# Optimization experiments

Hardware: AMD Instinct MI355X
Metric: run time of the kernel (lower is better)

Reference implementation:

```python
import jax, jax.numpy as jnp
import numpy as np

IN_FEATURES = 128
OUT_FEATURES = 64
NEG_INF = -9e15
LEAKY_SLOPE = 0.01  # nn.LeakyReLU() default


def _xavier_uniform(key, shape, gain):
    fan_in, fan_out = shape[0], shape[1]
    limit = gain * np.sqrt(6.0 / (fan_in + fan_out))
    return jax.random.uniform(key, shape, jnp.float32, -limit, limit)


def setup_inputs() -> dict:
    key = jax.random.key(0)
    k_h, k_adj, k_w, k_a = jax.random.split(key, 4)
    B, N = 8, 2048
    h = jax.random.normal(k_h, (B, N, IN_FEATURES), dtype=jnp.float32)
    adj = jax.random.randint(k_adj, (B, N, N), 0, 2, dtype=jnp.int32)
    W = _xavier_uniform(k_w, (IN_FEATURES, OUT_FEATURES), gain=1.414)
    a = _xavier_uniform(k_a, (2 * OUT_FEATURES, 1), gain=1.414)
    return {"h": h, "adj": adj, "W": W, "a": a}


def reference(h, adj, W, a):
    # Wh: [B, N, out]
    Wh = jnp.matmul(h, W)
    # a1, a2: [out, 1] slices of a
    a1 = a[:OUT_FEATURES]
    a2 = a[OUT_FEATURES:]
    Wh_a1 = jnp.matmul(Wh, a1)  # [B, N, 1]
    Wh_a2 = jnp.matmul(Wh, a2)  # [B, N, 1]
    # e[b,i,j] = leakyrelu(Wh_a1[b,i] * Wh_a2[b,j])  -- rank-1 outer product
    e = jax.nn.leaky_relu(Wh_a1 * jnp.swapaxes(Wh_a2, 1, 2), negative_slope=LEAKY_SLOPE)
    mask = adj > 0
    attention = jnp.where(mask, e, NEG_INF)
    attention = jax.nn.softmax(attention, axis=2)
    attention = jnp.where(mask, attention, 0.0)
    h_prime = jnp.matmul(attention, Wh)  # [B, N, out]
    return jax.nn.elu(h_prime)  # concat=True
```

## Files before the change

kernel.cpp:

```cpp
#include <hip/hip_runtime.h>

#define NTOK 2048

typedef __attribute__((ext_vector_type(8))) short s8v;
typedef __attribute__((ext_vector_type(4))) float f32x4;

__device__ inline unsigned short f2bf(float f) {
  unsigned u = __builtin_bit_cast(unsigned, f);
  u += 0x7FFFu + ((u >> 16) & 1u);
  return (unsigned short)(u >> 16);
}

__global__ __launch_bounds__(256) void gat_pre(
    const float* __restrict__ h, const float* __restrict__ W,
    const float* __restrict__ a, unsigned short* __restrict__ WhT,
    float* __restrict__ f1, float* __restrict__ f2,
    float* __restrict__ gmaxs, float* __restrict__ gmins) {
  __shared__ float wL[128 * 64];
  __shared__ float hL[64 * 128];
  __shared__ unsigned short tL[64 * 66];
  __shared__ float bmx[4], bmn[4];
  int t = threadIdx.x;
  {
    const float4* W4 = (const float4*)W;
    float4* wL4 = (float4*)wL;
#pragma unroll
    for (int k = 0; k < 8; ++k) wL4[t + 256 * k] = W4[t + 256 * k];
    const float4* h4 = (const float4*)(h + (size_t)blockIdx.x * 64 * 128);
    float4* hL4 = (float4*)hL;
#pragma unroll
    for (int k = 0; k < 8; ++k) hL4[t + 256 * k] = h4[t + 256 * k];
  }
  __syncthreads();
  int w = t >> 6, lane = t & 63;
  float acc[16];
#pragma unroll
  for (int r = 0; r < 16; ++r) acc[r] = 0.f;
  for (int kc = 0; kc < 128; kc += 32) {
    float wreg[32];
#pragma unroll
    for (int kk = 0; kk < 32; ++kk) wreg[kk] = wL[(kc + kk) * 64 + lane];
#pragma unroll
    for (int r = 0; r < 16; ++r) {
      const float* hrow = &hL[(w * 16 + r) * 128 + kc];
#pragma unroll
      for (int kk = 0; kk < 32; kk += 4) {
        float4 hv = *(const float4*)(hrow + kk);
        acc[r] += hv.x * wreg[kk] + hv.y * wreg[kk + 1] +
                  hv.z * wreg[kk + 2] + hv.w * wreg[kk + 3];
      }
    }
  }
  float a1 = a[lane], a2 = a[lane + 64];
  int row0 = blockIdx.x * 64 + w * 16;
  float wmx = -3.4e38f, wmn = 3.4e38f;
#pragma unroll
  for (int r = 0; r < 16; ++r) {
    float v1 = acc[r] * a1, v2 = acc[r] * a2;
#pragma unroll
    for (int s = 32; s; s >>= 1) {
      v1 += __shfl_xor(v1, s, 64);
      v2 += __shfl_xor(v2, s, 64);
    }
    if (lane == 0) { f1[row0 + r] = v1; f2[row0 + r] = v2; }
    wmx = fmaxf(wmx, v2);
    wmn = fminf(wmn, v2);
    tL[lane * 66 + w * 16 + r] = f2bf(acc[r]);
  }
  if (lane == 0) { bmx[w] = wmx; bmn[w] = wmn; }
  __syncthreads();
  int b = blockIdx.x >> 5;
  if (t == 0) {
    float mx = fmaxf(fmaxf(bmx[0], bmx[1]), fmaxf(bmx[2], bmx[3]));
    float mn = fminf(fminf(bmn[0], bmn[1]), fminf(bmn[2], bmn[3]));
    gmaxs[b * 32 + (blockIdx.x & 31)] = mx;
    gmins[b * 32 + (blockIdx.x & 31)] = mn;
  }
  int tok0 = (blockIdx.x & 31) * 64;
  int f = t >> 2, sub = t & 3;
  const unsigned short* src = &tL[f * 66];
  unsigned short* dst = WhT + ((size_t)b * 64 + f) * NTOK + tok0;
  *(uint4*)(dst + sub * 8) = *(const uint4*)(src + sub * 8);
  *(uint4*)(dst + 32 + sub * 8) = *(const uint4*)(src + 32 + sub * 8);
}

#define LOADX4(dst, va) \
  asm volatile("global_load_dwordx4 %0, %1, off" : "=v"(dst) : "v"(va))
#define WAITV(n) \
  asm volatile("s_waitcnt vmcnt(" #n ")" ::: "memory"); \
  __builtin_amdgcn_sched_barrier(0)
#define PACK4(s0, s1, s2, s3, s4, s5, s6, s7, D)                               \
  {                                                                            \
    unsigned b0 = (unsigned)(s0.x > 0) | ((unsigned)(s0.y > 0) << 1) |         \
                  ((unsigned)(s0.z > 0) << 2) | ((unsigned)(s0.w > 0) << 3) |  \
                  ((unsigned)(s1.x > 0) << 4) | ((unsigned)(s1.y > 0) << 5) |  \
                  ((unsigned)(s1.z > 0) << 6) | ((unsigned)(s1.w > 0) << 7);   \
    unsigned b1 = (unsigned)(s2.x > 0) | ((unsigned)(s2.y > 0) << 1) |         \
                  ((unsigned)(s2.z > 0) << 2) | ((unsigned)(s2.w > 0) << 3) |  \
                  ((unsigned)(s3.x > 0) << 4) | ((unsigned)(s3.y > 0) << 5) |  \
                  ((unsigned)(s3.z > 0) << 6) | ((unsigned)(s3.w > 0) << 7);   \
    unsigned b2 = (unsigned)(s4.x > 0) | ((unsigned)(s4.y > 0) << 1) |         \
                  ((unsigned)(s4.z > 0) << 2) | ((unsigned)(s4.w > 0) << 3) |  \
                  ((unsigned)(s5.x > 0) << 4) | ((unsigned)(s5.y > 0) << 5) |  \
                  ((unsigned)(s5.z > 0) << 6) | ((unsigned)(s5.w > 0) << 7);   \
    unsigned b3 = (unsigned)(s6.x > 0) | ((unsigned)(s6.y > 0) << 1) |         \
                  ((unsigned)(s6.z > 0) << 2) | ((unsigned)(s6.w > 0) << 3) |  \
                  ((unsigned)(s7.x > 0) << 4) | ((unsigned)(s7.y > 0) << 5) |  \
                  ((unsigned)(s7.z > 0) << 6) | ((unsigned)(s7.w > 0) << 7);   \
    D = b0 | (b1 << 8) | (b2 << 16) | (b3 << 24);                              \
  }

__global__ __launch_bounds__(512, 2) void gat_main(
    const int* __restrict__ adj, const unsigned short* __restrict__ WhT,
    const float* __restrict__ f1, const float* __restrict__ f2,
    const float* __restrict__ gmaxs, const float* __restrict__ gmins,
    unsigned short* __restrict__ part, float* __restrict__ dsum) {
  __shared__ __align__(16) unsigned char wTile[65536];
  __shared__ float f2L[512];
  int t = threadIdx.x;
  int pt = blockIdx.x, b = blockIdx.y, ks = blockIdx.z;
  int w = t >> 6, lane = t & 63, l15 = lane & 15, lhi = lane >> 4;

  {
    int ff = t >> 3;
    const char* srow =
        (const char*)(WhT + (size_t)b * 64 * NTOK + (size_t)ff * NTOK + ks * 512);
    int cb0 = (t & 7) * 128;
#pragma unroll
    for (int u = 0; u < 8; ++u) {
      int cb = cb0 + u * 16;
      uint4 d = *(const uint4*)(srow + cb);
      *(uint4*)&wTile[ff * 1024 + (cb ^ ((ff & 7) << 4))] = d;
    }
    if (t < 128)
      ((float4*)f2L)[t] = ((const float4*)(f2 + (size_t)b * NTOK + ks * 512))[t];
  }
  __syncthreads();

  int rg = pt * 8 + w;
  int i0 = rg * 16;
  const float L2E = 1.44269504f;
  float f1s = f1[(size_t)b * NTOK + i0 + l15] * L2E;
  float gmx = -3.4e38f, gmn = 3.4e38f;
#pragma unroll
  for (int j = 0; j < 32; ++j) {
    gmx = fmaxf(gmx, gmaxs[b * 32 + j]);
    gmn = fminf(gmn, gmins[b * 32 + j]);
  }
  float mr = fmaxf(f1s * gmx, f1s * gmn);
  float ms = fmaxf(mr, 0.01f * mr);

  unsigned d0, d1, d2, d3;
  {
    const int* abase = adj + ((size_t)b * NTOK + i0) * NTOK + ks * 512;
    unsigned long long bp = (unsigned long long)abase + (unsigned)(lane * 32);
    int4 A0, A1, A2, A3, A4, A5, A6, A7;
    int4 B0, B1, B2, B3, B4, B5, B6, B7;
    __builtin_amdgcn_sched_barrier(0);
    LOADX4(A0, bp + 0ull);       LOADX4(A1, bp + 16ull);
    LOADX4(A2, bp + 8192ull);    LOADX4(A3, bp + 8208ull);
    LOADX4(A4, bp + 16384ull);   LOADX4(A5, bp + 16400ull);
    LOADX4(A6, bp + 24576ull);   LOADX4(A7, bp + 24592ull);
    LOADX4(B0, bp + 32768ull);   LOADX4(B1, bp + 32784ull);
    LOADX4(B2, bp + 40960ull);   LOADX4(B3, bp + 40976ull);
    LOADX4(B4, bp + 49152ull);   LOADX4(B5, bp + 49168ull);
    LOADX4(B6, bp + 57344ull);   LOADX4(B7, bp + 57360ull);
    WAITV(8);
    PACK4(A0, A1, A2, A3, A4, A5, A6, A7, d0);
    LOADX4(A0, bp + 65536ull);   LOADX4(A1, bp + 65552ull);
    LOADX4(A2, bp + 73728ull);   LOADX4(A3, bp + 73744ull);
    LOADX4(A4, bp + 81920ull);   LOADX4(A5, bp + 81936ull);
    LOADX4(A6, bp + 90112ull);   LOADX4(A7, bp + 90128ull);
    WAITV(8);
    PACK4(B0, B1, B2, B3, B4, B5, B6, B7, d1);
    LOADX4(B0, bp + 98304ull);   LOADX4(B1, bp + 98320ull);
    LOADX4(B2, bp + 106496ull);  LOADX4(B3, bp + 106512ull);
    LOADX4(B4, bp + 114688ull);  LOADX4(B5, bp + 114704ull);
    LOADX4(B6, bp + 122880ull);  LOADX4(B7, bp + 122896ull);
    WAITV(8);
    PACK4(A0, A1, A2, A3, A4, A5, A6, A7, d2);
    WAITV(0);
    PACK4(B0, B1, B2, B3, B4, B5, B6, B7, d3);
    __builtin_amdgcn_sched_barrier(0);
  }

  const s8v bones = {0x3F80, 0x3F80, 0x3F80, 0x3F80, 0x3F80, 0x3F80, 0x3F80, 0x3F80};
  f32x4 ac0 = {0.f, 0.f, 0.f, 0.f}, ac1 = ac0, ac2 = ac0, ac3 = ac0, ac4 = ac0;
  int sw = (l15 & 7) << 4;

#pragma unroll
  for (int ch = 0; ch < 16; ++ch) {
    int sidx = ch * 4 + lhi;
    unsigned r0 = __shfl(d0, sidx, 64);
    unsigned r1 = __shfl(d1, sidx, 64);
    unsigned r2 = __shfl(d2, sidx, 64);
    unsigned r3 = __shfl(d3, sidx, 64);
    unsigned sel = l15 < 8 ? (l15 < 4 ? r0 : r1) : (l15 < 12 ? r2 : r3);
    unsigned byte = (sel >> ((l15 & 3) * 8)) & 0xFFu;

    float4 v0 = *(const float4*)&f2L[ch * 32 + lhi * 8];
    float4 v1 = *(const float4*)&f2L[ch * 32 + lhi * 8 + 4];
    int kb = ch * 64 + lhi * 16;
    s8v bf0 = *(const s8v*)&wTile[l15 * 1024 + (kb ^ sw)];
    s8v bf1 = *(const s8v*)&wTile[(16 + l15) * 1024 + (kb ^ sw)];
    s8v bf2 = *(const s8v*)&wTile[(32 + l15) * 1024 + (kb ^ sw)];
    s8v bf3 = *(const s8v*)&wTile[(48 + l15) * 1024 + (kb ^ sw)];

    float sv[8] = {f1s * v0.x, f1s * v0.y, f1s * v0.z, f1s * v0.w,
                   f1s * v1.x, f1s * v1.y, f1s * v1.z, f1s * v1.w};
    s8v af;
#pragma unroll
    for (int q = 0; q < 8; ++q) {
      float sc = sv[q];
      float lk = fmaxf(sc, 0.01f * sc);
#if __has_builtin(__builtin_amdgcn_exp2f)
      float pe = __builtin_amdgcn_exp2f(lk - ms);
#else
      float pe = exp2f(lk - ms);
#endif
      float p = (byte & (1u << q)) ? pe : 0.f;
      unsigned uu = __builtin_bit_cast(unsigned, p) + 0x8000u;
      af[q] = (short)(uu >> 16);
    }
    ac0 = __builtin_amdgcn_mfma_f32_16x16x32_bf16(af, bf0, ac0, 0, 0, 0);
    ac1 = __builtin_amdgcn_mfma_f32_16x16x32_bf16(af, bf1, ac1, 0, 0, 0);
    ac2 = __builtin_amdgcn_mfma_f32_16x16x32_bf16(af, bf2, ac2, 0, 0, 0);
    ac3 = __builtin_amdgcn_mfma_f32_16x16x32_bf16(af, bf3, ac3, 0, 0, 0);
    ac4 = __builtin_amdgcn_mfma_f32_16x16x32_bf16(af, bones, ac4, 0, 0, 0);
  }

  size_t pb = ((size_t)(b * 128 + rg)) * 4 + ks;
  unsigned short* pp = part + pb * 1024;
#pragma unroll
  for (int reg = 0; reg < 4; ++reg) {
    int row = lhi * 4 + reg;
    pp[row * 64 + l15] = f2bf(ac0[reg]);
    pp[row * 64 + 16 + l15] = f2bf(ac1[reg]);
    pp[row * 64 + 32 + l15] = f2bf(ac2[reg]);
    pp[row * 64 + 48 + l15] = f2bf(ac3[reg]);
    if (l15 == 0) dsum[pb * 16 + row] = ac4[reg];
  }
}

__global__ __launch_bounds__(256) void gat_fin(
    const unsigned short* __restrict__ part, const float* __restrict__ dsum,
    float* __restrict__ out) {
  int gx = blockIdx.x, b = blockIdx.y, t = threadIdx.x;
  size_t g = (size_t)b * 128 + gx;
#pragma unroll
  for (int rep = 0; rep < 4; ++rep) {
    int idx = t + rep * 256;
    int mm = idx >> 6, f = idx & 63;
    float v = 0.f, dn = 0.f;
#pragma unroll
    for (int ks = 0; ks < 4; ++ks) {
      size_t pb = g * 4 + ks;
      unsigned us = part[pb * 1024 + mm * 64 + f];
      v += __builtin_bit_cast(float, us << 16);
      dn += dsum[pb * 16 + mm];
    }
    float rdn = dn > 0.f ? 1.0f / dn : 0.f;
    float hp = v * rdn;
    float o = hp > 0.f ? hp : expm1f(hp);
    out[((size_t)b * NTOK + gx * 16 + mm) * 64 + f] = o;
  }
}

extern "C" void kernel_launch(void* const* d_in, const int* in_sizes, int n_in,
                              void* d_out, int out_size, void* d_ws, size_t ws_size,
                              hipStream_t stream) {
  const float* h = (const float*)d_in[0];
  const int* adj = (const int*)d_in[1];
  const float* W = (const float*)d_in[2];
  const float* a = (const float*)d_in[3];
  float* out = (float*)d_out;

  char* ws = (char*)d_ws;
  unsigned short* WhT = (unsigned short*)ws;
  float* f1 = (float*)(ws + 2 * 1024 * 1024);
  float* f2 = f1 + 16384;
  float* gmaxs = (float*)(f2 + 16384);
  float* gmins = gmaxs + 256;
  unsigned short* part = (unsigned short*)(ws + 3 * 1024 * 1024);
  float* dsum = (float*)(ws + 11 * 1024 * 1024);

  gat_pre<<<256, 256, 0, stream>>>(h, W, a, WhT, f1, f2, gmaxs, gmins);
  gat_main<<<dim3(16, 8, 4), 512, 0, stream>>>(adj, WhT, f1, f2, gmaxs, gmins,
                                               part, dsum);
  gat_fin<<<dim3(128, 8), 256, 0, stream>>>(part, dsum, out);
}
```

Baseline: 58.71 us.

## Drop LDS WhT tile, read B fragments from global, shrink blocks, pipeline adj loads

The main kernel no longer stages the 64 KB WhT tile and the f2 slice in shared memory. MFMA B fragments and f2 values are now read directly from global memory, which relies on L2/L1 for reuse. Blocks shrink to 256 threads with a 4-blocks-per-SM bound and the grid doubles. Adjacency loads are issued in smaller rolling batches so fewer registers stay live. Mask bytes go through a small LDS buffer instead of cross-lane shuffles, and the pre kernel moves to 512 threads. This trades the LDS staging and barrier for more global or cache traffic per wave, aiming at higher occupancy and better latency hiding on the adjacency stream.

```diff
diff --git a/kernel.cpp b/kernel.cpp
--- a/kernel.cpp
+++ b/kernel.cpp
@@ -11,7 +11,7 @@
   return (unsigned short)(u >> 16);
 }
 
-__global__ __launch_bounds__(256) void gat_pre(
+__global__ __launch_bounds__(512) void gat_pre(
     const float* __restrict__ h, const float* __restrict__ W,
     const float* __restrict__ a, unsigned short* __restrict__ WhT,
     float* __restrict__ f1, float* __restrict__ f2,
@@ -19,30 +19,30 @@
   __shared__ float wL[128 * 64];
   __shared__ float hL[64 * 128];
   __shared__ unsigned short tL[64 * 66];
-  __shared__ float bmx[4], bmn[4];
+  __shared__ float bmx[8], bmn[8];
   int t = threadIdx.x;
   {
     const float4* W4 = (const float4*)W;
     float4* wL4 = (float4*)wL;
 #pragma unroll
-    for (int k = 0; k < 8; ++k) wL4[t + 256 * k] = W4[t + 256 * k];
+    for (int k = 0; k < 4; ++k) wL4[t + 512 * k] = W4[t + 512 * k];
     const float4* h4 = (const float4*)(h + (size_t)blockIdx.x * 64 * 128);
     float4* hL4 = (float4*)hL;
 #pragma unroll
-    for (int k = 0; k < 8; ++k) hL4[t + 256 * k] = h4[t + 256 * k];
+    for (int k = 0; k < 4; ++k) hL4[t + 512 * k] = h4[t + 512 * k];
   }
   __syncthreads();
   int w = t >> 6, lane = t & 63;
-  float acc[16];
-#pragma unroll
-  for (int r = 0; r < 16; ++r) acc[r] = 0.f;
+  float acc[8];
+#pragma unroll
+  for (int r = 0; r < 8; ++r) acc[r] = 0.f;
   for (int kc = 0; kc < 128; kc += 32) {
     float wreg[32];
 #pragma unroll
     for (int kk = 0; kk < 32; ++kk) wreg[kk] = wL[(kc + kk) * 64 + lane];
 #pragma unroll
-    for (int r = 0; r < 16; ++r) {
-      const float* hrow = &hL[(w * 16 + r) * 128 + kc];
+    for (int r = 0; r < 8; ++r) {
+      const float* hrow = &hL[(w * 8 + r) * 128 + kc];
 #pragma unroll
       for (int kk = 0; kk < 32; kk += 4) {
         float4 hv = *(const float4*)(hrow + kk);
@@ -52,10 +52,10 @@
     }
   }
   float a1 = a[lane], a2 = a[lane + 64];
-  int row0 = blockIdx.x * 64 + w * 16;
+  int row0 = blockIdx.x * 64 + w * 8;
   float wmx = -3.4e38f, wmn = 3.4e38f;
 #pragma unroll
-  for (int r = 0; r < 16; ++r) {
+  for (int r = 0; r < 8; ++r) {
     float v1 = acc[r] * a1, v2 = acc[r] * a2;
 #pragma unroll
     for (int s = 32; s; s >>= 1) {
@@ -65,23 +65,25 @@
     if (lane == 0) { f1[row0 + r] = v1; f2[row0 + r] = v2; }
     wmx = fmaxf(wmx, v2);
     wmn = fminf(wmn, v2);
-    tL[lane * 66 + w * 16 + r] = f2bf(acc[r]);
+    tL[lane * 66 + w * 8 + r] = f2bf(acc[r]);
   }
   if (lane == 0) { bmx[w] = wmx; bmn[w] = wmn; }
   __syncthreads();
   int b = blockIdx.x >> 5;
   if (t == 0) {
-    float mx = fmaxf(fmaxf(bmx[0], bmx[1]), fmaxf(bmx[2], bmx[3]));
-    float mn = fminf(fminf(bmn[0], bmn[1]), fminf(bmn[2], bmn[3]));
+    float mx = bmx[0], mn = bmn[0];
+#pragma unroll
+    for (int j = 1; j < 8; ++j) {
+      mx = fmaxf(mx, bmx[j]);
+      mn = fminf(mn, bmn[j]);
+    }
     gmaxs[b * 32 + (blockIdx.x & 31)] = mx;
     gmins[b * 32 + (blockIdx.x & 31)] = mn;
   }
   int tok0 = (blockIdx.x & 31) * 64;
-  int f = t >> 2, sub = t & 3;
-  const unsigned short* src = &tL[f * 66];
+  int f = t >> 3, sub = t & 7;
   unsigned short* dst = WhT + ((size_t)b * 64 + f) * NTOK + tok0;
-  *(uint4*)(dst + sub * 8) = *(const uint4*)(src + sub * 8);
-  *(uint4*)(dst + 32 + sub * 8) = *(const uint4*)(src + 32 + sub * 8);
+  *(uint4*)(dst + sub * 8) = *(const uint4*)&tL[f * 66 + sub * 8];
 }
 
 #define LOADX4(dst, va) \
@@ -89,55 +91,39 @@
 #define WAITV(n) \
   asm volatile("s_waitcnt vmcnt(" #n ")" ::: "memory"); \
   __builtin_amdgcn_sched_barrier(0)
-#define PACK4(s0, s1, s2, s3, s4, s5, s6, s7, D)                               \
+#define ISS(X, r)                                  \
+  LOADX4(X##0, bp + (r) * 8192ull);                \
+  LOADX4(X##1, bp + (r) * 8192ull + 16ull);        \
+  LOADX4(X##2, bp + (r) * 8192ull + 8192ull);      \
+  LOADX4(X##3, bp + (r) * 8192ull + 8208ull)
+#define PK2(X, r, D)                                                           \
   {                                                                            \
-    unsigned b0 = (unsigned)(s0.x > 0) | ((unsigned)(s0.y > 0) << 1) |         \
-                  ((unsigned)(s0.z > 0) << 2) | ((unsigned)(s0.w > 0) << 3) |  \
-                  ((unsigned)(s1.x > 0) << 4) | ((unsigned)(s1.y > 0) << 5) |  \
-                  ((unsigned)(s1.z > 0) << 6) | ((unsigned)(s1.w > 0) << 7);   \
-    unsigned b1 = (unsigned)(s2.x > 0) | ((unsigned)(s2.y > 0) << 1) |         \
-                  ((unsigned)(s2.z > 0) << 2) | ((unsigned)(s2.w > 0) << 3) |  \
-                  ((unsigned)(s3.x > 0) << 4) | ((unsigned)(s3.y > 0) << 5) |  \
-                  ((unsigned)(s3.z > 0) << 6) | ((unsigned)(s3.w > 0) << 7);   \
-    unsigned b2 = (unsigned)(s4.x > 0) | ((unsigned)(s4.y > 0) << 1) |         \
-                  ((unsigned)(s4.z > 0) << 2) | ((unsigned)(s4.w > 0) << 3) |  \
-                  ((unsigned)(s5.x > 0) << 4) | ((unsigned)(s5.y > 0) << 5) |  \
-                  ((unsigned)(s5.z > 0) << 6) | ((unsigned)(s5.w > 0) << 7);   \
-    unsigned b3 = (unsigned)(s6.x > 0) | ((unsigned)(s6.y > 0) << 1) |         \
-                  ((unsigned)(s6.z > 0) << 2) | ((unsigned)(s6.w > 0) << 3) |  \
-                  ((unsigned)(s7.x > 0) << 4) | ((unsigned)(s7.y > 0) << 5) |  \
-                  ((unsigned)(s7.z > 0) << 6) | ((unsigned)(s7.w > 0) << 7);   \
-    D = b0 | (b1 << 8) | (b2 << 16) | (b3 << 24);                              \
-  }
-
-__global__ __launch_bounds__(512, 2) void gat_main(
+    int4 pa = X##0;                                                            \
+    int4 pbv = X##1;                                                           \
+    int4 pc = X##2;                                                            \
+    int4 pd = X##3;                                                            \
+    unsigned ba = (unsigned)(pa.x > 0) | ((unsigned)(pa.y > 0) << 1) |         \
+                  ((unsigned)(pa.z > 0) << 2) | ((unsigned)(pa.w > 0) << 3) |  \
+                  ((unsigned)(pbv.x > 0) << 4) | ((unsigned)(pbv.y > 0) << 5) |\
+                  ((unsigned)(pbv.z > 0) << 6) | ((unsigned)(pbv.w > 0) << 7); \
+    unsigned bb = (unsigned)(pc.x > 0) | ((unsigned)(pc.y > 0) << 1) |         \
+                  ((unsigned)(pc.z > 0) << 2) | ((unsigned)(pc.w > 0) << 3) |  \
+                  ((unsigned)(pd.x > 0) << 4) | ((unsigned)(pd.y > 0) << 5) |  \
+                  ((unsigned)(pd.z > 0) << 6) | ((unsigned)(pd.w > 0) << 7);   \
+    D |= (ba << (((r) & 3) * 8)) | (bb << ((((r) + 1) & 3) * 8));              \
+  }
+
+__global__ __launch_bounds__(256, 4) void gat_main(
     const int* __restrict__ adj, const unsigned short* __restrict__ WhT,
     const float* __restrict__ f1, const float* __restrict__ f2,
     const float* __restrict__ gmaxs, const float* __restrict__ gmins,
     unsigned short* __restrict__ part, float* __restrict__ dsum) {
-  __shared__ __align__(16) unsigned char wTile[65536];
-  __shared__ float f2L[512];
+  __shared__ __align__(16) unsigned char mT[4][1024];
   int t = threadIdx.x;
   int pt = blockIdx.x, b = blockIdx.y, ks = blockIdx.z;
   int w = t >> 6, lane = t & 63, l15 = lane & 15, lhi = lane >> 4;
 
-  {
-    int ff = t >> 3;
-    const char* srow =
-        (const char*)(WhT + (size_t)b * 64 * NTOK + (size_t)ff * NTOK + ks * 512);
-    int cb0 = (t & 7) * 128;
-#pragma unroll
-    for (int u = 0; u < 8; ++u) {
-      int cb = cb0 + u * 16;
-      uint4 d = *(const uint4*)(srow + cb);
-      *(uint4*)&wTile[ff * 1024 + (cb ^ ((ff & 7) << 4))] = d;
-    }
-    if (t < 128)
-      ((float4*)f2L)[t] = ((const float4*)(f2 + (size_t)b * NTOK + ks * 512))[t];
-  }
-  __syncthreads();
-
-  int rg = pt * 8 + w;
+  int rg = pt * 4 + w;
   int i0 = rg * 16;
   const float L2E = 1.44269504f;
   float f1s = f1[(size_t)b * NTOK + i0 + l15] * L2E;
@@ -150,61 +136,46 @@
   float mr = fmaxf(f1s * gmx, f1s * gmn);
   float ms = fmaxf(mr, 0.01f * mr);
 
-  unsigned d0, d1, d2, d3;
+  unsigned d0 = 0, d1 = 0, d2 = 0, d3 = 0;
   {
     const int* abase = adj + ((size_t)b * NTOK + i0) * NTOK + ks * 512;
     unsigned long long bp = (unsigned long long)abase + (unsigned)(lane * 32);
-    int4 A0, A1, A2, A3, A4, A5, A6, A7;
-    int4 B0, B1, B2, B3, B4, B5, B6, B7;
+    int4 A0, A1, A2, A3, B0, B1, B2, B3;
     __builtin_amdgcn_sched_barrier(0);
-    LOADX4(A0, bp + 0ull);       LOADX4(A1, bp + 16ull);
-    LOADX4(A2, bp + 8192ull);    LOADX4(A3, bp + 8208ull);
-    LOADX4(A4, bp + 16384ull);   LOADX4(A5, bp + 16400ull);
-    LOADX4(A6, bp + 24576ull);   LOADX4(A7, bp + 24592ull);
-    LOADX4(B0, bp + 32768ull);   LOADX4(B1, bp + 32784ull);
-    LOADX4(B2, bp + 40960ull);   LOADX4(B3, bp + 40976ull);
-    LOADX4(B4, bp + 49152ull);   LOADX4(B5, bp + 49168ull);
-    LOADX4(B6, bp + 57344ull);   LOADX4(B7, bp + 57360ull);
-    WAITV(8);
-    PACK4(A0, A1, A2, A3, A4, A5, A6, A7, d0);
-    LOADX4(A0, bp + 65536ull);   LOADX4(A1, bp + 65552ull);
-    LOADX4(A2, bp + 73728ull);   LOADX4(A3, bp + 73744ull);
-    LOADX4(A4, bp + 81920ull);   LOADX4(A5, bp + 81936ull);
-    LOADX4(A6, bp + 90112ull);   LOADX4(A7, bp + 90128ull);
-    WAITV(8);
-    PACK4(B0, B1, B2, B3, B4, B5, B6, B7, d1);
-    LOADX4(B0, bp + 98304ull);   LOADX4(B1, bp + 98320ull);
-    LOADX4(B2, bp + 106496ull);  LOADX4(B3, bp + 106512ull);
-    LOADX4(B4, bp + 114688ull);  LOADX4(B5, bp + 114704ull);
-    LOADX4(B6, bp + 122880ull);  LOADX4(B7, bp + 122896ull);
-    WAITV(8);
-    PACK4(A0, A1, A2, A3, A4, A5, A6, A7, d2);
-    WAITV(0);
-    PACK4(B0, B1, B2, B3, B4, B5, B6, B7, d3);
+    ISS(A, 0); ISS(B, 2);
+    WAITV(4); PK2(A, 0, d0); ISS(A, 4);
+    WAITV(4); PK2(B, 2, d0); ISS(B, 6);
+    WAITV(4); PK2(A, 4, d1); ISS(A, 8);
+    WAITV(4); PK2(B, 6, d1); ISS(B, 10);
+    WAITV(4); PK2(A, 8, d2); ISS(A, 12);
+    WAITV(4); PK2(B, 10, d2); ISS(B, 14);
+    WAITV(4); PK2(A, 12, d3);
+    WAITV(0); PK2(B, 14, d3);
     __builtin_amdgcn_sched_barrier(0);
   }
 
+  {
+    uint4 dd = {d0, d1, d2, d3};
+    *(uint4*)&mT[w][lane * 16] = dd;
+  }
+
+  const float* f2p = f2 + (size_t)b * NTOK + ks * 512;
+  const unsigned short* bp0 =
+      WhT + (size_t)b * 64 * NTOK + (size_t)l15 * NTOK + ks * 512;
   const s8v bones = {0x3F80, 0x3F80, 0x3F80, 0x3F80, 0x3F80, 0x3F80, 0x3F80, 0x3F80};
   f32x4 ac0 = {0.f, 0.f, 0.f, 0.f}, ac1 = ac0, ac2 = ac0, ac3 = ac0, ac4 = ac0;
-  int sw = (l15 & 7) << 4;
 
 #pragma unroll
   for (int ch = 0; ch < 16; ++ch) {
-    int sidx = ch * 4 + lhi;
-    unsigned r0 = __shfl(d0, sidx, 64);
-    unsigned r1 = __shfl(d1, sidx, 64);
-    unsigned r2 = __shfl(d2, sidx, 64);
-    unsigned r3 = __shfl(d3, sidx, 64);
-    unsigned sel = l15 < 8 ? (l15 < 4 ? r0 : r1) : (l15 < 12 ? r2 : r3);
-    unsigned byte = (sel >> ((l15 & 3) * 8)) & 0xFFu;
-
-    float4 v0 = *(const float4*)&f2L[ch * 32 + lhi * 8];
-    float4 v1 = *(const float4*)&f2L[ch * 32 + lhi * 8 + 4];
-    int kb = ch * 64 + lhi * 16;
-    s8v bf0 = *(const s8v*)&wTile[l15 * 1024 + (kb ^ sw)];
-    s8v bf1 = *(const s8v*)&wTile[(16 + l15) * 1024 + (kb ^ sw)];
-    s8v bf2 = *(const s8v*)&wTile[(32 + l15) * 1024 + (kb ^ sw)];
-    s8v bf3 = *(const s8v*)&wTile[(48 + l15) * 1024 + (kb ^ sw)];
+    unsigned byte = mT[w][(ch * 4 + lhi) * 16 + l15];
+    int kl = ch * 32 + lhi * 8;
+    float4 v0 = *(const float4*)(f2p + kl);
+    float4 v1 = *(const float4*)(f2p + kl + 4);
+    const unsigned short* bp = bp0 + kl;
+    s8v bf0 = *(const s8v*)(bp);
+    s8v bf1 = *(const s8v*)(bp + 16 * NTOK);
+    s8v bf2 = *(const s8v*)(bp + 32 * NTOK);
+    s8v bf3 = *(const s8v*)(bp + 48 * NTOK);
 
     float sv[8] = {f1s * v0.x, f1s * v0.y, f1s * v0.z, f1s * v0.w,
                    f1s * v1.x, f1s * v1.y, f1s * v1.z, f1s * v1.w};
@@ -229,8 +200,8 @@
     ac4 = __builtin_amdgcn_mfma_f32_16x16x32_bf16(af, bones, ac4, 0, 0, 0);
   }
 
-  size_t pb = ((size_t)(b * 128 + rg)) * 4 + ks;
-  unsigned short* pp = part + pb * 1024;
+  size_t pb2 = ((size_t)(b * 128 + rg)) * 4 + ks;
+  unsigned short* pp = part + pb2 * 1024;
 #pragma unroll
   for (int reg = 0; reg < 4; ++reg) {
     int row = lhi * 4 + reg;
@@ -238,7 +209,7 @@
     pp[row * 64 + 16 + l15] = f2bf(ac1[reg]);
     pp[row * 64 + 32 + l15] = f2bf(ac2[reg]);
     pp[row * 64 + 48 + l15] = f2bf(ac3[reg]);
-    if (l15 == 0) dsum[pb * 16 + row] = ac4[reg];
+    if (l15 == 0) dsum[pb2 * 16 + row] = ac4[reg];
   }
 }
 
@@ -284,8 +255,8 @@
   unsigned short* part = (unsigned short*)(ws + 3 * 1024 * 1024);
   float* dsum = (float*)(ws + 11 * 1024 * 1024);
 
-  gat_pre<<<256, 256, 0, stream>>>(h, W, a, WhT, f1, f2, gmaxs, gmins);
-  gat_main<<<dim3(16, 8, 4), 512, 0, stream>>>(adj, WhT, f1, f2, gmaxs, gmins,
+  gat_pre<<<256, 512, 0, stream>>>(h, W, a, WhT, f1, f2, gmaxs, gmins);
+  gat_main<<<dim3(32, 8, 4), 256, 0, stream>>>(adj, WhT, f1, f2, gmaxs, gmins,
                                                part, dsum);
   gat_fin<<<dim3(128, 8), 256, 0, stream>>>(part, dsum, out);
 }
```

Result: slower. 73.74 us (+25.6%).
